# Performance work log

Hardware: AMD Instinct MI355X
Metric: run time of the kernel (lower is better)

## Reference

```python
import jax, jax.numpy as jnp
import numpy as np
import math

N_EMBD = 1024
N_HEAD = 16
HEAD_DIM = N_EMBD // N_HEAD
B, T = 2, 2048
LORA_RANK = 16      # 8-bit setting
LORA_SCALE = 32.0 / 16.0  # alpha / rank
QMIN, QMAX = 0.0, 255.0   # 8-bit asymmetric


def round_ste(x):
    return x + jax.lax.stop_gradient(jnp.round(x) - x)


def fake_quant(x, scale, zero_point):
    # LearnableFakeQuantize, asymmetric 8-bit, straight-through round
    q = jnp.clip(round_ste(x / scale + zero_point), QMIN, QMAX)
    return (q - zero_point) * scale


def lora_linear(x, w, b, la, lb):
    # base linear + LoRA path (dropout disabled / eval)
    return x @ w + b + LORA_SCALE * ((x @ la) @ lb)


def setup_inputs() -> dict:
    key = jax.random.key(0)
    ks = jax.random.split(key, 10)
    std = 0.02
    hidden_states = jax.random.normal(ks[0], (B, T, N_EMBD), dtype=jnp.float32)
    w_attn = jax.random.normal(ks[1], (N_EMBD, 3 * N_EMBD), dtype=jnp.float32) * std
    b_attn = jnp.zeros((3 * N_EMBD,), dtype=jnp.float32)
    la_attn = jax.random.normal(ks[2], (N_EMBD, LORA_RANK), dtype=jnp.float32) * std
    lb_attn = jnp.zeros((LORA_RANK, 3 * N_EMBD), dtype=jnp.float32)
    w_proj = jax.random.normal(ks[3], (N_EMBD, N_EMBD), dtype=jnp.float32) * std
    b_proj = jnp.zeros((N_EMBD,), dtype=jnp.float32)
    la_proj = jax.random.normal(ks[4], (N_EMBD, LORA_RANK), dtype=jnp.float32) * std
    lb_proj = jnp.zeros((LORA_RANK, N_EMBD), dtype=jnp.float32)
    kv_scale = jnp.asarray(0.05, dtype=jnp.float32)
    kv_zero_point = jnp.asarray(128.0, dtype=jnp.float32)
    return {
        'hidden_states': hidden_states,
        'w_attn': w_attn, 'b_attn': b_attn, 'la_attn': la_attn, 'lb_attn': lb_attn,
        'w_proj': w_proj, 'b_proj': b_proj, 'la_proj': la_proj, 'lb_proj': lb_proj,
        'kv_scale': kv_scale, 'kv_zero_point': kv_zero_point,
    }


def reference(hidden_states, w_attn, b_attn, la_attn, lb_attn,
              w_proj, b_proj, la_proj, lb_proj, kv_scale, kv_zero_point):
    Bn, Tn, C = hidden_states.shape
    qkv = lora_linear(hidden_states, w_attn, b_attn, la_attn, lb_attn)
    q, k, v = jnp.split(qkv, 3, axis=2)
    # [B, T, C] -> [B, H, T, D]
    def to_heads(x):
        return x.reshape(Bn, Tn, N_HEAD, HEAD_DIM).transpose(0, 2, 1, 3)
    q, k, v = to_heads(q), to_heads(k), to_heads(v)
    k = fake_quant(k, kv_scale, kv_zero_point)
    v = fake_quant(v, kv_scale, kv_zero_point)
    scores = jnp.einsum('bhqd,bhkd->bhqk', q, k) / math.sqrt(HEAD_DIM)
    causal = jnp.tril(jnp.ones((Tn, Tn), dtype=bool))
    scores = jnp.where(causal, scores, -jnp.inf)
    attn = jax.nn.softmax(scores, axis=-1)
    out = jnp.einsum('bhqk,bhkd->bhqd', attn, v)
    out = out.transpose(0, 2, 1, 3).reshape(Bn, Tn, C)
    return lora_linear(out, w_proj, b_proj, la_proj, lb_proj)
```

## Files before the change

### kernel.cpp

```cpp
#include <hip/hip_runtime.h>
#include <hip/hip_bf16.h>
#include <math.h>

#define N_EMBD   1024
#define N_HEAD   16
#define HEAD_DIM 64
#define BATCH    2
#define TSEQ     2048
#define RANK     16
#define LORA_SCALE 2.0f
#define M_TOTAL  (BATCH * TSEQ)
#define C3       (3 * N_EMBD)

typedef unsigned short ushort_t;
typedef __attribute__((ext_vector_type(8))) short bf16x8;
typedef __attribute__((ext_vector_type(4))) float f32x4;

__device__ __forceinline__ float fake_quant(float x, float scale, float zp) {
    float q = rintf(x / scale + zp);
    q = fminf(fmaxf(q, 0.0f), 255.0f);
    return (q - zp) * scale;
}

__device__ __forceinline__ ushort_t bf16bits(float f) {
    union { __hip_bfloat16 h; ushort_t u; } c;
    c.h = __float2bfloat16(f);
    return c.u;
}

__device__ __forceinline__ float bfraw2f(ushort_t u) {
    union { unsigned int i; float f; } c; c.i = ((unsigned int)u) << 16; return c.f;
}

#define NB_LORA 1024
#define NB_TRA  3072
#define NB_TRP  1024
#define NB_CVT  4096

__device__ __forceinline__ void transpose_body(
        const float* __restrict__ in, __hip_bfloat16* __restrict__ hiT,
        __hip_bfloat16* __restrict__ loT, int R, int C,
        int c0, int r0, int tid, float* sh) {
    float (*tl)[33] = (float(*)[33])sh;
    const int tx = tid & 31, ty = tid >> 5;
    for (int i = ty; i < 32; i += 8)
        tl[i][tx] = in[(size_t)(r0 + i) * C + c0 + tx];
    __syncthreads();
    for (int i = ty; i < 32; i += 8) {
        float v = tl[tx][i];
        __hip_bfloat16 h = __float2bfloat16(v);
        size_t o = (size_t)(c0 + i) * R + r0 + tx;
        hiT[o] = h;
        if (loT) loT[o] = __float2bfloat16(v - __bfloat162float(h));
    }
}

__global__ __launch_bounds__(256)
void prep_kernel(const float* __restrict__ x,
                 const float* __restrict__ w_attn,
                 const float* __restrict__ w_proj,
                 const float* __restrict__ la_attn,
                 __hip_bfloat16* __restrict__ x_hi,
                 __hip_bfloat16* __restrict__ x_lo,
                 __hip_bfloat16* __restrict__ wqT_h,
                 __hip_bfloat16* __restrict__ wqT_l,
                 __hip_bfloat16* __restrict__ wpT,
                 float* __restrict__ t_attn_p) {
    __shared__ float sh[33 * 32];
    const int tid = threadIdx.x;
    int b = blockIdx.x;

    if (b < NB_LORA) {
        const int bx = b & 255, by = b >> 8;
        float (*Xs)[64] = (float(*)[64])sh;
        const int ty = tid >> 4, tx = tid & 15;
        const int row0 = bx * 16;
        const int kbase = by * 256;
        float acc = 0.0f;
        for (int k0 = kbase; k0 < kbase + 256; k0 += 64) {
            int rr = tid >> 4, kk = (tid & 15) * 4;
            float4 v = *(const float4*)(x + (size_t)(row0 + rr) * N_EMBD + k0 + kk);
            Xs[rr][kk] = v.x; Xs[rr][kk + 1] = v.y; Xs[rr][kk + 2] = v.z; Xs[rr][kk + 3] = v.w;
            __syncthreads();
            for (int k = 0; k < 64; ++k)
                acc += Xs[ty][k] * la_attn[(size_t)(k0 + k) * RANK + tx];
            __syncthreads();
        }
        t_attn_p[((size_t)by * M_TOTAL + row0 + ty) * RANK + tx] = acc;
        return;
    }
    b -= NB_LORA;
    if (b < NB_TRA) {
        const int gx = b % (C3 / 32), gy = b / (C3 / 32);
        transpose_body(w_attn, wqT_h, wqT_l, N_EMBD, C3, gx * 32, gy * 32, tid, sh);
        return;
    }
    b -= NB_TRA;
    if (b < NB_TRP) {
        const int gx = b & 31, gy = b >> 5;
        transpose_body(w_proj, wpT, nullptr, N_EMBD, N_EMBD, gx * 32, gy * 32, tid, sh);
        return;
    }
    b -= NB_TRP;
    {
        const int i = b * 256 + tid;
        float4 v = ((const float4*)x)[i];
        float vs[4] = {v.x, v.y, v.z, v.w};
        #pragma unroll
        for (int k = 0; k < 4; ++k) {
            __hip_bfloat16 h = __float2bfloat16(vs[k]);
            x_hi[i * 4 + k] = h;
            x_lo[i * 4 + k] = __float2bfloat16(vs[k] - __bfloat162float(h));
        }
    }
}

__global__ void vtrans_kernel(const ushort_t* __restrict__ Vb,
                              ushort_t* __restrict__ Vt) {
    __shared__ ushort_t tl[64][68];
    const int bh = blockIdx.x & 31, tt = blockIdx.x >> 5;
    const int tid = threadIdx.x;
    {
        const int t = tid >> 2, d0 = (tid & 3) * 16;
        const uint4 u = *(const uint4*)(Vb + ((size_t)bh * TSEQ + tt * 64 + t) * 64 + d0);
        *(uint4*)&tl[t][d0] = u;
        *(uint4*)&tl[t][d0 + 8] = *(const uint4*)(Vb + ((size_t)bh * TSEQ + tt * 64 + t) * 64 + d0 + 8);
    }
    __syncthreads();
    const int d = tid >> 2, t0 = (tid & 3) * 16;
    unsigned int wbuf[8];
    #pragma unroll
    for (int j = 0; j < 8; ++j)
        wbuf[j] = (unsigned int)tl[t0 + 2 * j][d] | ((unsigned int)tl[t0 + 2 * j + 1][d] << 16);
    ushort_t* dst = Vt + ((size_t)bh * 64 + d) * TSEQ + tt * 64 + t0;
    *(uint4*)dst       = make_uint4(wbuf[0], wbuf[1], wbuf[2], wbuf[3]);
    *(uint4*)(dst + 8) = make_uint4(wbuf[4], wbuf[5], wbuf[6], wbuf[7]);
}

__global__ void lora_t_part_bf16_kernel(const ushort_t* __restrict__ x,
                                        const float* __restrict__ la,
                                        float* __restrict__ tpart, int K) {
    __shared__ float Xs[16][64];
    const int tid = threadIdx.x;
    const int ty = tid >> 4, tx = tid & 15;
    const int row0 = blockIdx.x * 16;
    const int kbase = blockIdx.y * 256;
    float acc = 0.0f;
    for (int k0 = kbase; k0 < kbase + 256; k0 += 64) {
        int rr = tid >> 4, kk = (tid & 15) * 4;
        const ushort4 u = *(const ushort4*)(x + (size_t)(row0 + rr) * K + k0 + kk);
        Xs[rr][kk] = bfraw2f(u.x); Xs[rr][kk + 1] = bfraw2f(u.y);
        Xs[rr][kk + 2] = bfraw2f(u.z); Xs[rr][kk + 3] = bfraw2f(u.w);
        __syncthreads();
        for (int k = 0; k < 64; ++k)
            acc += Xs[ty][k] * la[(size_t)(k0 + k) * RANK + tx];
        __syncthreads();
    }
    tpart[((size_t)blockIdx.y * M_TOTAL + row0 + ty) * RANK + tx] = acc;
}

__device__ __forceinline__ int sw_off(int r, int c) {
    return ((r >> 1) << 7) + (((((r & 1) << 2) | c) ^ ((r >> 1) & 7)) << 4);
}

template <bool SPLIT, int TM>
__global__ __launch_bounds__(256, 3)
void gemm_mfma_kernel(const __hip_bfloat16* __restrict__ Ah,
                      const __hip_bfloat16* __restrict__ Al,
                      const __hip_bfloat16* __restrict__ Bh,
                      const __hip_bfloat16* __restrict__ Bl,
                      const float* __restrict__ bias,
                      const float* __restrict__ tpart,
                      const float* __restrict__ lb,
                      float* __restrict__ Cf,
                      ushort_t* __restrict__ Qb,
                      ushort_t* __restrict__ Kb,
                      ushort_t* __restrict__ Vb,
                      const float* __restrict__ sp,
                      const float* __restrict__ zp,
                      int M, int N, int K, int split_col0, int out_mode) {
    constexpr int TILEA = TM * 32;
    constexpr int TILEB = 128 * 32;
    constexpr int MI = TM / 32;
    __shared__ __align__(16) __hip_bfloat16 As[3 * TILEA];
    __shared__ __align__(16) __hip_bfloat16 Bs[3 * TILEB];
    float* Ts = (float*)As;
    float* Ls = (float*)Bs;

    const int tid = threadIdx.x;
    const int lane = tid & 63, w = tid >> 6;

    int bcol, brow;
    {
        const int NC = gridDim.x, NR = gridDim.y;
        const int lid = blockIdx.y * NC + blockIdx.x;
        const int xcd = lid & 7, s = lid >> 3;
        const int cw = NC >> 1, rh = NR >> 2;
        const int cg = xcd & 1, rg = xcd >> 1;
        if (SPLIT) {
            bcol = 2 * (s % cw) + cg;
            brow = rg * rh + (s / cw);
        } else {
            bcol = cg * cw + (s % cw);
            brow = rg * rh + (s / cw);
        }
    }
    const int row0 = brow * TM, col0 = bcol * 128;
    const int wr = (w >> 1) * (TM >> 1), wc = (w & 1) * 64;
    const bool do_split = SPLIT && (col0 >= split_col0);

    const int s_lc = (lane & 7) ^ ((lane >> 3) & 7);
    const int s_rb = 2 * (lane >> 3) + (s_lc >> 2);
    const int s_c8 = (s_lc & 3) * 8;

    float qsc = 0.f, qzp = 0.f;
    if (out_mode == 1) { qsc = sp[0]; qzp = zp[0]; }

    f32x4 acc[MI][4];
    #pragma unroll
    for (int i = 0; i < MI; ++i)
        #pragma unroll
        for (int j = 0; j < 4; ++j)
            acc[i][j] = (f32x4){0.f, 0.f, 0.f, 0.f};

    const int arow = wr + (lane & 15);
    const int chunk = lane >> 4;

    const ushort_t* alp[4];
    const ushort_t* blp[4];
    if (do_split) {
        #pragma unroll
        for (int mi = 0; mi < MI; ++mi)
            alp[mi] = (const ushort_t*)Al + (size_t)(row0 + arow + mi * 16) * K + chunk * 8;
        #pragma unroll
        for (int nj = 0; nj < 4; ++nj)
            blp[nj] = (const ushort_t*)Bl + (size_t)(col0 + wc + nj * 16 + (lane & 15)) * K + chunk * 8;
    }

    auto stage = [&](int buf, int kidx) {
        const int k0 = kidx << 5;
        __hip_bfloat16* dA = As + buf * TILEA;
        __hip_bfloat16* dB = Bs + buf * TILEB;
        if (TM == 128) {
            #pragma unroll
            for (int qq = 0; qq < 2; ++qq) {
                const int q = 2 * w + qq;
                const int r = 16 * q + s_rb;
                const __hip_bfloat16* gA = Ah + (size_t)(row0 + r) * K + k0 + s_c8;
                __builtin_amdgcn_global_load_lds(
                    (const __attribute__((address_space(1))) void*)gA,
                    (__attribute__((address_space(3))) void*)(dA + q * 512), 16, 0, 0);
                const __hip_bfloat16* gB = Bh + (size_t)(col0 + r) * K + k0 + s_c8;
                __builtin_amdgcn_global_load_lds(
                    (const __attribute__((address_space(1))) void*)gB,
                    (__attribute__((address_space(3))) void*)(dB + q * 512), 16, 0, 0);
            }
        } else {
            const int rA = 16 * w + s_rb;
            const __hip_bfloat16* gA = Ah + (size_t)(row0 + rA) * K + k0 + s_c8;
            __builtin_amdgcn_global_load_lds(
                (const __attribute__((address_space(1))) void*)gA,
                (__attribute__((address_space(3))) void*)(dA + w * 512), 16, 0, 0);
            #pragma unroll
            for (int qq = 0; qq < 2; ++qq) {
                const int q = 2 * w + qq;
                const int r = 16 * q + s_rb;
                const __hip_bfloat16* gB = Bh + (size_t)(col0 + r) * K + k0 + s_c8;
                __builtin_amdgcn_global_load_lds(
                    (const __attribute__((address_space(1))) void*)gB,
                    (__attribute__((address_space(3))) void*)(dB + q * 512), 16, 0, 0);
            }
        }
    };

    const int KI = K >> 5;
    stage(0, 0);
    stage(1, 1);
    int bcur = 0, bstage = 2;
    for (int kk = 0; kk < KI; ++kk) {
        if (kk == KI - 1) {
            asm volatile("s_waitcnt vmcnt(0)" ::: "memory");
        } else if (TM == 128) {
            asm volatile("s_waitcnt vmcnt(4)" ::: "memory");
        } else {
            asm volatile("s_waitcnt vmcnt(3)" ::: "memory");
        }
        __builtin_amdgcn_s_barrier();

        const int k0 = kk << 5;
        bf16x8 a_l[MI], b_l[4];
        if (do_split) {
            #pragma unroll
            for (int mi = 0; mi < MI; ++mi) a_l[mi] = *(const bf16x8*)(alp[mi] + k0);
            #pragma unroll
            for (int nj = 0; nj < 4; ++nj) b_l[nj] = *(const bf16x8*)(blp[nj] + k0);
        }
        if (kk + 2 < KI) { stage(bstage, kk + 2); bstage = (bstage == 2) ? 0 : bstage + 1; }

        const char* ab = (const char*)(As + bcur * TILEA);
        const char* bb = (const char*)(Bs + bcur * TILEB);
        bf16x8 a_h[MI], b_h[4];
        #pragma unroll
        for (int mi = 0; mi < MI; ++mi)
            a_h[mi] = *(const bf16x8*)(ab + sw_off(arow + mi * 16, chunk));
        #pragma unroll
        for (int nj = 0; nj < 4; ++nj)
            b_h[nj] = *(const bf16x8*)(bb + sw_off(wc + nj * 16 + (lane & 15), chunk));
        #pragma unroll
        for (int mi = 0; mi < MI; ++mi)
            #pragma unroll
            for (int nj = 0; nj < 4; ++nj)
                acc[mi][nj] = __builtin_amdgcn_mfma_f32_16x16x32_bf16(a_h[mi], b_h[nj], acc[mi][nj], 0, 0, 0);
        if (do_split) {
            #pragma unroll
            for (int mi = 0; mi < MI; ++mi)
                #pragma unroll
                for (int nj = 0; nj < 4; ++nj) {
                    acc[mi][nj] = __builtin_amdgcn_mfma_f32_16x16x32_bf16(a_h[mi], b_l[nj], acc[mi][nj], 0, 0, 0);
                    acc[mi][nj] = __builtin_amdgcn_mfma_f32_16x16x32_bf16(a_l[mi], b_h[nj], acc[mi][nj], 0, 0, 0);
                }
        }
        bcur = (bcur == 2) ? 0 : bcur + 1;
    }
    __syncthreads();

    {
        int r = tid >> 1, j0 = (tid & 1) * 8;
        if (r < TM) {
            float4 t0 = {0, 0, 0, 0}, t1 = {0, 0, 0, 0};
            #pragma unroll
            for (int c = 0; c < 4; ++c) {
                const float* src = tpart + ((size_t)c * M_TOTAL + row0 + r) * RANK + j0;
                float4 s0 = *(const float4*)src;
                float4 s1 = *(const float4*)(src + 4);
                t0.x += s0.x; t0.y += s0.y; t0.z += s0.z; t0.w += s0.w;
                t1.x += s1.x; t1.y += s1.y; t1.z += s1.z; t1.w += s1.w;
            }
            *(float4*)(Ts + r * 16 + j0)     = t0;
            *(float4*)(Ts + r * 16 + j0 + 4) = t1;
        }
        int rr = tid >> 4, c0 = (tid & 15) * 8;
        const float4* lsrc = (const float4*)(lb + (size_t)rr * N + col0 + c0);
        float4* ldst = (float4*)(Ls + rr * 128 + c0);
        ldst[0] = lsrc[0]; ldst[1] = lsrc[1];
    }
    __syncthreads();
    #pragma unroll
    for (int mi = 0; mi < MI; ++mi)
        #pragma unroll
        for (int nj = 0; nj < 4; ++nj) {
            const int coll = wc + nj * 16 + (lane & 15);
            const float bv = bias[col0 + coll];
            #pragma unroll
            for (int rg = 0; rg < 4; ++rg) {
                const int rowl = wr + mi * 16 + (lane >> 4) * 4 + rg;
                float lsum = 0.f;
                #pragma unroll
                for (int rr = 0; rr < 16; ++rr)
                    lsum += Ts[rowl * 16 + rr] * Ls[rr * 128 + coll];
                const float val = acc[mi][nj][rg] + bv + LORA_SCALE * lsum;
                if (out_mode == 0) {
                    Cf[(size_t)(row0 + rowl) * N + col0 + coll] = val;
                } else {
                    const int R = row0 + rowl;
                    const int b = R >> 11, t = R & 2047;
                    const int CN = col0 + coll;
                    const int sec = CN >> 10, head = (CN >> 6) & 15, d = CN & 63;
                    const size_t off = (((size_t)(b * 16 + head)) * TSEQ + t) * 64 + d;
                    if (sec == 0)      Qb[off] = bf16bits(val * 0.125f);
                    else if (sec == 1) Kb[off] = bf16bits(fake_quant(val, qsc, qzp));
                    else               Vb[off] = bf16bits(fake_quant(val, qsc, qzp));
                }
            }
        }
}

__global__ __launch_bounds__(256)
void mfma_attn_kernel(const ushort_t* __restrict__ Qb,
                      const ushort_t* __restrict__ Kq,
                      const ushort_t* __restrict__ Vtq,
                      ushort_t* __restrict__ outb) {
    const int bx = blockIdx.x;
    const int bh = bx & 31;
    const int qt = 31 - (bx >> 5);
    const int b = bh >> 4, h = bh & 15;
    const int tid = threadIdx.x;
    const int lane = tid & 63, w = tid >> 6;
    const int m16 = lane & 15, qc = lane >> 4;
    const int m7 = m16 & 7;

    __shared__ ushort_t Qs[4096];
    __shared__ ushort_t Ks[2][4096];
    __shared__ ushort_t Vs[2][4096];
    __shared__ ushort_t Ps[4096];

    const int s_g = (lane & 7) ^ ((lane >> 3) & 7);
    const int s_r = lane >> 3;

    const ushort_t* Qg = Qb + (size_t)bh * TSEQ * 64;
    const ushort_t* Kg = Kq + (size_t)bh * TSEQ * 64;
    const ushort_t* Vg = Vtq + (size_t)bh * 64 * TSEQ;

    auto stageKV = [&](int buf, int kt) {
        #pragma unroll
        for (int pp = 0; pp < 2; ++pp) {
            const int p = 2 * w + pp;
            const ushort_t* gk = Kg + ((size_t)(kt * 64 + 8 * p + s_r)) * 64 + s_g * 8;
            __builtin_amdgcn_global_load_lds(
                (const __attribute__((address_space(1))) void*)gk,
                (__attribute__((address_space(3))) void*)(Ks[buf] + p * 512), 16, 0, 0);
            const ushort_t* gv = Vg + ((size_t)(8 * p + s_r)) * TSEQ + kt * 64 + s_g * 8;
            __builtin_amdgcn_global_load_lds(
                (const __attribute__((address_space(1))) void*)gv,
                (__attribute__((address_space(3))) void*)(Vs[buf] + p * 512), 16, 0, 0);
        }
    };

    #pragma unroll
    for (int pp = 0; pp < 2; ++pp) {
        const int p = 2 * w + pp;
        const ushort_t* gq = Qg + ((size_t)(qt * 64 + 8 * p + s_r)) * 64 + s_g * 8;
        __builtin_amdgcn_global_load_lds(
            (const __attribute__((address_space(1))) void*)gq,
            (__attribute__((address_space(3))) void*)(Qs + p * 512), 16, 0, 0);
    }
    stageKV(0, 0);
    __syncthreads();

    bf16x8 a_q[2];
    {
        const int row = 16 * w + m16;
        #pragma unroll
        for (int c = 0; c < 2; ++c) {
            const int g = qc + 4 * c;
            a_q[c] = *(const bf16x8*)((const char*)Qs + row * 128 + ((g ^ m7) << 4));
        }
    }

    float m_st[4], l_st[4];
    f32x4 o_acc[4];
    #pragma unroll
    for (int r = 0; r < 4; ++r) { m_st[r] = -INFINITY; l_st[r] = 0.0f; }
    #pragma unroll
    for (int dj = 0; dj < 4; ++dj) o_acc[dj] = (f32x4){0.f, 0.f, 0.f, 0.f};

    for (int kt = 0; kt <= qt; ++kt) {
        const int cur = kt & 1;
        if (kt < qt) {
            stageKV(cur ^ 1, kt + 1);
            asm volatile("s_waitcnt vmcnt(4)" ::: "memory");
        } else {
            asm volatile("s_waitcnt vmcnt(0)" ::: "memory");
        }
        __builtin_amdgcn_s_barrier();

        const bool diag = (kt == qt);
        const int nj_hi = diag ? (w + 1) : 4;

        f32x4 s[4];
        #pragma unroll
        for (int nj = 0; nj < 4; ++nj) s[nj] = (f32x4){0.f, 0.f, 0.f, 0.f};
        #pragma unroll
        for (int c = 0; c < 2; ++c) {
            #pragma unroll
            for (int nj = 0; nj < 4; ++nj) {
                if (nj < nj_hi) {
                    const int row = 16 * nj + m16;
                    const int g = qc + 4 * c;
                    bf16x8 bk = *(const bf16x8*)((const char*)Ks[cur] + row * 128 + ((g ^ m7) << 4));
                    s[nj] = __builtin_amdgcn_mfma_f32_16x16x32_bf16(a_q[c], bk, s[nj], 0, 0, 0);
                }
            }
        }

        float alpha[4], p_[4][4];
        #pragma unroll
        for (int reg = 0; reg < 4; ++reg) {
            const int qrow = 16 * w + 4 * qc + reg;
            float sv[4];
            float rm = -INFINITY;
            #pragma unroll
            for (int nj = 0; nj < 4; ++nj) {
                float v = s[nj][reg];
                if (diag && (m16 + 16 * nj > qrow)) v = -INFINITY;
                sv[nj] = v;
                rm = fmaxf(rm, v);
            }
            #pragma unroll
            for (int off = 1; off < 16; off <<= 1)
                rm = fmaxf(rm, __shfl_xor(rm, off, 16));
            const float mo = m_st[reg];
            const float mn = fmaxf(mo, rm);
            const float al = __expf(mo - mn);
            float rs = 0.f;
            #pragma unroll
            for (int nj = 0; nj < 4; ++nj) {
                float pv = __expf(sv[nj] - mn);
                p_[reg][nj] = pv;
                rs += pv;
            }
            #pragma unroll
            for (int off = 1; off < 16; off <<= 1)
                rs += __shfl_xor(rs, off, 16);
            l_st[reg] = al * l_st[reg] + rs;
            m_st[reg] = mn;
            alpha[reg] = al;
        }

        #pragma unroll
        for (int reg = 0; reg < 4; ++reg) {
            const int row = 16 * w + 4 * qc + reg;
            const int r7 = row & 7;
            #pragma unroll
            for (int nj = 0; nj < 4; ++nj) {
                const int k = m16 + 16 * nj;
                Ps[row * 64 + (((k >> 3) ^ r7) << 3) + (k & 7)] = bf16bits(p_[reg][nj]);
            }
        }

        #pragma unroll
        for (int dj = 0; dj < 4; ++dj)
            #pragma unroll
            for (int reg = 0; reg < 4; ++reg)
                o_acc[dj][reg] *= alpha[reg];

        const int c_hi = diag ? (w >= 2 ? 2 : 1) : 2;
        #pragma unroll
        for (int c = 0; c < 2; ++c) {
            if (c < c_hi) {
                const int rowp = 16 * w + m16;
                const int g = qc + 4 * c;
                bf16x8 ap = *(const bf16x8*)((const char*)Ps + rowp * 128 + ((g ^ m7) << 4));
                #pragma unroll
                for (int dj = 0; dj < 4; ++dj) {
                    const int rowv = 16 * dj + m16;
                    bf16x8 bv = *(const bf16x8*)((const char*)Vs[cur] + rowv * 128 + ((g ^ m7) << 4));
                    o_acc[dj] = __builtin_amdgcn_mfma_f32_16x16x32_bf16(ap, bv, o_acc[dj], 0, 0, 0);
                }
            }
        }
        asm volatile("s_barrier" ::: "memory");
    }

    #pragma unroll
    for (int reg = 0; reg < 4; ++reg) {
        const float inv = 1.0f / l_st[reg];
        const int q = qt * 64 + 16 * w + 4 * qc + reg;
        #pragma unroll
        for (int dj = 0; dj < 4; ++dj) {
            const int d = m16 + 16 * dj;
            outb[((size_t)b * TSEQ + q) * N_EMBD + h * 64 + d] = bf16bits(o_acc[dj][reg] * inv);
        }
    }
}

extern "C" void kernel_launch(void* const* d_in, const int* in_sizes, int n_in,
                              void* d_out, int out_size, void* d_ws, size_t ws_size,
                              hipStream_t stream) {
    const float* x        = (const float*)d_in[0];
    const float* w_attn   = (const float*)d_in[1];
    const float* b_attn   = (const float*)d_in[2];
    const float* la_attn  = (const float*)d_in[3];
    const float* lb_attn  = (const float*)d_in[4];
    const float* w_proj   = (const float*)d_in[5];
    const float* b_proj   = (const float*)d_in[6];
    const float* la_proj  = (const float*)d_in[7];
    const float* lb_proj  = (const float*)d_in[8];
    const float* kv_scale = (const float*)d_in[9];
    const float* kv_zp    = (const float*)d_in[10];
    float* out = (float*)d_out;

    char* ws = (char*)d_ws;
    float* t_attn_p       = (float*)ws;          ws += (size_t)4 * M_TOTAL * RANK * 4;
    float* t_proj_p       = (float*)ws;          ws += (size_t)4 * M_TOTAL * RANK * 4;
    ushort_t* aob         = (ushort_t*)ws;       ws += (size_t)M_TOTAL * N_EMBD * 2;
    __hip_bfloat16* x_hi  = (__hip_bfloat16*)ws; ws += (size_t)M_TOTAL * N_EMBD * 2;
    __hip_bfloat16* x_lo  = (__hip_bfloat16*)ws; ws += (size_t)M_TOTAL * N_EMBD * 2;
    __hip_bfloat16* wqT_h = (__hip_bfloat16*)ws; ws += (size_t)C3 * N_EMBD * 2;
    __hip_bfloat16* wqT_l = (__hip_bfloat16*)ws; ws += (size_t)C3 * N_EMBD * 2;
    __hip_bfloat16* wpT   = (__hip_bfloat16*)ws; ws += (size_t)N_EMBD * N_EMBD * 2;
    ushort_t* Qb          = (ushort_t*)ws;       ws += (size_t)32 * TSEQ * 64 * 2;
    ushort_t* Kb          = (ushort_t*)ws;       ws += (size_t)32 * TSEQ * 64 * 2;
    ushort_t* Vb          = (ushort_t*)ws;       ws += (size_t)32 * TSEQ * 64 * 2;
    ushort_t* Vtq         = (ushort_t*)ws;       ws += (size_t)32 * 64 * TSEQ * 2;

    prep_kernel<<<dim3(NB_LORA + NB_TRA + NB_TRP + NB_CVT), 256, 0, stream>>>(
        x, w_attn, w_proj, la_attn,
        x_hi, x_lo, wqT_h, wqT_l, wpT, t_attn_p);

    gemm_mfma_kernel<true, 128><<<dim3(24, 32), 256, 0, stream>>>(
        x_hi, x_lo, wqT_h, wqT_l, b_attn, t_attn_p, lb_attn,
        nullptr, Qb, Kb, Vb, kv_scale, kv_zp,
        M_TOTAL, C3, N_EMBD, 2 * N_EMBD, 1);

    vtrans_kernel<<<dim3(32 * (TSEQ / 64)), 256, 0, stream>>>(Vb, Vtq);

    mfma_attn_kernel<<<dim3(32 * 32), 256, 0, stream>>>(Qb, Kb, Vtq, aob);

    lora_t_part_bf16_kernel<<<dim3(M_TOTAL / 16, 4), 256, 0, stream>>>(aob, la_proj, t_proj_p, N_EMBD);

    gemm_mfma_kernel<false, 64><<<dim3(8, 64), 256, 0, stream>>>(
        (const __hip_bfloat16*)aob, nullptr, wpT, nullptr, b_proj, t_proj_p, lb_proj,
        out, nullptr, nullptr, nullptr, nullptr, nullptr,
        M_TOTAL, N_EMBD, N_EMBD, 1 << 30, 0);
}
```

Baseline: 297.0 us.

## Shrink QKV GEMM tile to 64 rows with double buffering and drop Q LDS staging

The QKV GEMM now runs with 64-row tiles, a two-buffer LDS pipeline and a larger grid. Launch bounds on the GEMM and attention kernels are raised to 4 blocks per CU to increase occupancy. The attention kernel now loads Q fragments straight from global memory into registers, which removes the Q shared-memory buffer and one barrier. The cost is a shallower prefetch pipeline with an extra barrier per k-step in the GEMM, possible register pressure from the tighter launch bounds, and uncoalesced Q loads.

```diff
diff --git a/kernel.cpp b/kernel.cpp
--- a/kernel.cpp
+++ b/kernel.cpp
@@ -163,8 +163,8 @@
     return ((r >> 1) << 7) + (((((r & 1) << 2) | c) ^ ((r >> 1) & 7)) << 4);
 }
 
-template <bool SPLIT, int TM>
-__global__ __launch_bounds__(256, 3)
+template <bool SPLIT, int TM, int NBUF>
+__global__ __launch_bounds__(256, 4)
 void gemm_mfma_kernel(const __hip_bfloat16* __restrict__ Ah,
                       const __hip_bfloat16* __restrict__ Al,
                       const __hip_bfloat16* __restrict__ Bh,
@@ -182,8 +182,9 @@
     constexpr int TILEA = TM * 32;
     constexpr int TILEB = 128 * 32;
     constexpr int MI = TM / 32;
-    __shared__ __align__(16) __hip_bfloat16 As[3 * TILEA];
-    __shared__ __align__(16) __hip_bfloat16 Bs[3 * TILEB];
+    constexpr int SLOADS = (TM == 128) ? 4 : 3;
+    __shared__ __align__(16) __hip_bfloat16 As[NBUF * TILEA];
+    __shared__ __align__(16) __hip_bfloat16 Bs[NBUF * TILEB];
     float* Ts = (float*)As;
     float* Ls = (float*)Bs;
 
@@ -226,7 +227,7 @@
     const int arow = wr + (lane & 15);
     const int chunk = lane >> 4;
 
-    const ushort_t* alp[4];
+    const ushort_t* alp[MI];
     const ushort_t* blp[4];
     if (do_split) {
         #pragma unroll
@@ -274,13 +275,17 @@
     };
 
     const int KI = K >> 5;
-    stage(0, 0);
-    stage(1, 1);
-    int bcur = 0, bstage = 2;
+    int bcur = 0, bstage;
+    if (NBUF == 3) { stage(0, 0); stage(1, 1); bstage = 2; }
+    else           { stage(0, 0); bstage = 1; }
+
     for (int kk = 0; kk < KI; ++kk) {
+        if (NBUF == 2) {
+            if (kk + 1 < KI) stage(bstage, kk + 1);
+        }
         if (kk == KI - 1) {
             asm volatile("s_waitcnt vmcnt(0)" ::: "memory");
-        } else if (TM == 128) {
+        } else if (SLOADS == 4) {
             asm volatile("s_waitcnt vmcnt(4)" ::: "memory");
         } else {
             asm volatile("s_waitcnt vmcnt(3)" ::: "memory");
@@ -295,7 +300,9 @@
             #pragma unroll
             for (int nj = 0; nj < 4; ++nj) b_l[nj] = *(const bf16x8*)(blp[nj] + k0);
         }
-        if (kk + 2 < KI) { stage(bstage, kk + 2); bstage = (bstage == 2) ? 0 : bstage + 1; }
+        if (NBUF == 3) {
+            if (kk + 2 < KI) { stage(bstage, kk + 2); bstage = (bstage == 2) ? 0 : bstage + 1; }
+        }
 
         const char* ab = (const char*)(As + bcur * TILEA);
         const char* bb = (const char*)(Bs + bcur * TILEB);
@@ -320,7 +327,12 @@
                     acc[mi][nj] = __builtin_amdgcn_mfma_f32_16x16x32_bf16(a_l[mi], b_h[nj], acc[mi][nj], 0, 0, 0);
                 }
         }
-        bcur = (bcur == 2) ? 0 : bcur + 1;
+        if (NBUF == 2) {
+            asm volatile("s_waitcnt lgkmcnt(0)\ns_barrier" ::: "memory");
+            bcur ^= 1; bstage ^= 1;
+        } else {
+            bcur = (bcur == 2) ? 0 : bcur + 1;
+        }
     }
     __syncthreads();
 
@@ -375,7 +387,7 @@
         }
 }
 
-__global__ __launch_bounds__(256)
+__global__ __launch_bounds__(256, 4)
 void mfma_attn_kernel(const ushort_t* __restrict__ Qb,
                       const ushort_t* __restrict__ Kq,
                       const ushort_t* __restrict__ Vtq,
@@ -389,7 +401,6 @@
     const int m16 = lane & 15, qc = lane >> 4;
     const int m7 = m16 & 7;
 
-    __shared__ ushort_t Qs[4096];
     __shared__ ushort_t Ks[2][4096];
     __shared__ ushort_t Vs[2][4096];
     __shared__ ushort_t Ps[4096];
@@ -416,25 +427,13 @@
         }
     };
 
-    #pragma unroll
-    for (int pp = 0; pp < 2; ++pp) {
-        const int p = 2 * w + pp;
-        const ushort_t* gq = Qg + ((size_t)(qt * 64 + 8 * p + s_r)) * 64 + s_g * 8;
-        __builtin_amdgcn_global_load_lds(
-            (const __attribute__((address_space(1))) void*)gq,
-            (__attribute__((address_space(3))) void*)(Qs + p * 512), 16, 0, 0);
-    }
     stageKV(0, 0);
-    __syncthreads();
 
     bf16x8 a_q[2];
     {
-        const int row = 16 * w + m16;
-        #pragma unroll
-        for (int c = 0; c < 2; ++c) {
-            const int g = qc + 4 * c;
-            a_q[c] = *(const bf16x8*)((const char*)Qs + row * 128 + ((g ^ m7) << 4));
-        }
+        const ushort_t* qrow = Qg + (size_t)(qt * 64 + 16 * w + m16) * 64;
+        a_q[0] = *(const bf16x8*)(qrow + qc * 8);
+        a_q[1] = *(const bf16x8*)(qrow + (qc + 4) * 8);
     }
 
     float m_st[4], l_st[4];
@@ -588,7 +587,7 @@
         x, w_attn, w_proj, la_attn,
         x_hi, x_lo, wqT_h, wqT_l, wpT, t_attn_p);
 
-    gemm_mfma_kernel<true, 128><<<dim3(24, 32), 256, 0, stream>>>(
+    gemm_mfma_kernel<true, 64, 2><<<dim3(24, 64), 256, 0, stream>>>(
         x_hi, x_lo, wqT_h, wqT_l, b_attn, t_attn_p, lb_attn,
         nullptr, Qb, Kb, Vb, kv_scale, kv_zp,
         M_TOTAL, C3, N_EMBD, 2 * N_EMBD, 1);
@@ -599,7 +598,7 @@
 
     lora_t_part_bf16_kernel<<<dim3(M_TOTAL / 16, 4), 256, 0, stream>>>(aob, la_proj, t_proj_p, N_EMBD);
 
-    gemm_mfma_kernel<false, 64><<<dim3(8, 64), 256, 0, stream>>>(
+    gemm_mfma_kernel<false, 64, 3><<<dim3(8, 64), 256, 0, stream>>>(
         (const __hip_bfloat16*)aob, nullptr, wpT, nullptr, b_proj, t_proj_p, lb_proj,
         out, nullptr, nullptr, nullptr, nullptr, nullptr,
         M_TOTAL, N_EMBD, N_EMBD, 1 << 30, 0);
```

After: 411.2 us. +38.5%, slower.
